# Kernel tuning notes

Hardware: AMD Instinct MI355X
Metric: run time of the kernel (lower is better)

## Reference

```python
import jax, jax.numpy as jnp
import numpy as np

B, N_C, N_F = 2, 16384, 65536          # batch, coarse nodes, fine (up_nodes)
C_IN, C_OUT = 128, 128
E_C, E_F = 65536, 262144               # coarse / fine edge counts


def _mlp_params(key, cin, cout):
    # 2-layer MLP (Linear-ReLU-Linear) + LayerNorm, torch default uniform init
    k1, k2 = jax.random.split(key)
    s1 = 1.0 / np.sqrt(2 * cin)
    s2 = 1.0 / np.sqrt(cout)
    W1 = jax.random.uniform(k1, (2 * cin, cout), minval=-s1, maxval=s1, dtype=jnp.float32)
    W2 = jax.random.uniform(k2, (cout, cout), minval=-s2, maxval=s2, dtype=jnp.float32)
    return (W1, jnp.zeros((cout,), jnp.float32), W2, jnp.zeros((cout,), jnp.float32),
            jnp.ones((cout,), jnp.float32), jnp.zeros((cout,), jnp.float32))


def setup_inputs() -> dict:
    key = jax.random.key(0)
    rng = np.random.default_rng(0)
    x = jax.random.normal(jax.random.fold_in(key, 1), (B, N_C, C_IN), dtype=jnp.float32)
    # sorted unique unpool indices (m_id)
    idx = jnp.asarray(np.sort(rng.choice(N_F, N_C, replace=False)).astype(np.int64))
    ei_c = jnp.asarray(rng.integers(0, N_C, size=(2, E_C)).astype(np.int64))
    ei_f = jnp.asarray(rng.integers(0, N_F, size=(2, E_F)).astype(np.int64))
    d = {"x": x, "idx": idx, "ei_c": ei_c, "ei_f": ei_f}
    for pre, k, cin, cout in (("s", 2, C_IN, C_OUT), ("a", 3, C_IN, C_OUT // 2), ("b", 4, C_OUT // 2, C_OUT)):
        W1, b1, W2, b2, g, bt = _mlp_params(jax.random.fold_in(key, k), cin, cout)
        d.update({pre + "W1": W1, pre + "b1": b1, pre + "W2": W2, pre + "b2": b2, pre + "g": g, pre + "bt": bt})
    return d


def _unpool(x, idx, n):
    # scatter coarse features into a zero-filled fine array (Unpool module)
    return jnp.zeros((x.shape[0], n, x.shape[-1]), x.dtype).at[:, idx].set(x)


def _edgeconv(x, ei, W1, b1, W2, b2, g, bt, n):
    # EdgeConv: aggregate_sum over edges of MLP([x_i, x_j - x_i]) + LayerNorm
    src, dst = ei[0], ei[1]
    xd = x[:, dst]                                   # [B,E,cin] gather at target
    feat = jnp.concatenate([xd, x[:, src] - xd], axis=-1)  # [B,E,2*cin]
    h = jax.nn.relu(feat @ W1 + b1) @ W2 + b2        # [B,E,cout]
    mu = jnp.mean(h, axis=-1, keepdims=True)
    var = jnp.var(h, axis=-1, keepdims=True)
    h = (h - mu) * jax.lax.rsqrt(var + 1e-5) * g + bt
    return jax.vmap(lambda hb: jax.ops.segment_sum(hb, dst, num_segments=n))(h)


def reference(x, idx, ei_c, ei_f,
              sW1, sb1, sW2, sb2, sg, sbt,
              aW1, ab1, aW2, ab2, ag, abt,
              bW1, bb1, bW2, bb2, bg, bbt):
    # skip branch: unpool then EdgeConv cin->cout on fine graph
    skip = _edgeconv(_unpool(x, idx, N_F), ei_f, sW1, sb1, sW2, sb2, sg, sbt, N_F)
    # main branch: EdgeConv cin->cout/2 on coarse, unpool, EdgeConv cout/2->cout on fine
    h = _edgeconv(x, ei_c, aW1, ab1, aW2, ab2, ag, abt, N_C)
    h = _edgeconv(_unpool(h, idx, N_F), ei_f, bW1, bb1, bW2, bb2, bg, bbt, N_F)
    return jax.nn.leaky_relu(h + skip, 0.01)
```

## Files before the change

kernel.cpp:

```cpp
#include <hip/hip_runtime.h>

typedef _Float16 half8  __attribute__((ext_vector_type(8)));
typedef _Float16 half4v __attribute__((ext_vector_type(4)));
typedef _Float16 half2v __attribute__((ext_vector_type(2)));
typedef float    f32x4  __attribute__((ext_vector_type(4)));
typedef float    f32x2  __attribute__((ext_vector_type(2)));
typedef int      i32x4  __attribute__((ext_vector_type(4)));

#define NB 2
#define N_C 16384
#define N_F 65536
#define E_C 65536
#define E_F 262144

#define INV4  ((size_t)N_F / 4)
#define CNT4  ((size_t)(N_F + N_C) / 4)

__global__ void clear_small(int* __restrict__ inv, int* __restrict__ cnt) {
    size_t i = (size_t)blockIdx.x * 256 + threadIdx.x;
    const i32x4 z = {0, 0, 0, 0};
    const i32x4 m1 = {-1, -1, -1, -1};
    if (i < INV4) ((i32x4*)inv)[i] = m1;
    else if (i < INV4 + CNT4) ((i32x4*)cnt)[i - INV4] = z;
}

__device__ inline void swizzle_dev(const float* __restrict__ W, _Float16* __restrict__ Ws,
                                   int N, int o) {
    int j = o & 7;
    int lane = (o >> 3) & 63;
    int frag = o >> 9;
    int ntiles = N >> 4;
    int nt = frag % ntiles;
    int kt = frag / ntiles;
    int k = kt * 32 + (lane >> 4) * 8 + j;
    int n = nt * 16 + (lane & 15);
    Ws[o] = (_Float16)W[k * N + n];
}

__device__ inline void swz_node(const float* __restrict__ W, _Float16* __restrict__ Ws,
                                int CIN, int COUT, int o) {
    int j = o & 7;
    int lane = (o >> 3) & 63;
    int frag = o >> 9;
    int N2 = 2 * COUT;
    int ntiles = N2 >> 4;
    int nt = frag % ntiles;
    int kt = frag / ntiles;
    int k = kt * 32 + (lane >> 4) * 8 + j;
    int n = nt * 16 + (lane & 15);
    float v = (n < COUT) ? W[k * COUT + n] - W[(k + CIN) * COUT + n]
                         : W[(k + CIN) * COUT + (n - COUT)];
    Ws[o] = (_Float16)v;
}

__global__ void setup_all(const int* __restrict__ idx, int* __restrict__ inv,
                          const float* sW1, const float* sW2, const float* aW1,
                          const float* aW2, const float* bW1, const float* bW2,
                          const float* sb1, const float* ab1, const float* bb1,
                          _Float16* sW1n, _Float16* sW2s, _Float16* aW1n,
                          _Float16* aW2s, _Float16* bW1n, _Float16* bW2s,
                          _Float16* b1h,
                          const int* __restrict__ ei_f, const int* __restrict__ ei_c,
                          int* __restrict__ cnt) {
    const int bb = blockIdx.x, t = threadIdx.x;
    if (bb < 64) {
        int i = bb * 256 + t;
        inv[idx[i]] = i;
    } else if (bb < 192) {
        swz_node(sW1, sW1n, 128, 128, (bb - 64) * 256 + t);
    } else if (bb < 256) {
        swizzle_dev(sW2, sW2s, 128, (bb - 192) * 256 + t);
    } else if (bb < 320) {
        swz_node(aW1, aW1n, 128, 64, (bb - 256) * 256 + t);
    } else if (bb < 336) {
        swizzle_dev(aW2, aW2s, 64, (bb - 320) * 256 + t);
    } else if (bb < 400) {
        swz_node(bW1, bW1n, 64, 128, (bb - 336) * 256 + t);
    } else if (bb < 464) {
        swizzle_dev(bW2, bW2s, 128, (bb - 400) * 256 + t);
    } else if (bb < 466) {
        int i = (bb - 464) * 256 + t;
        if (i < 128) b1h[i] = (_Float16)sb1[i];
        else if (i < 192) b1h[i] = (_Float16)ab1[i - 128];
        else if (i < 320) b1h[i] = (_Float16)bb1[i - 192];
    } else if (bb < 1490) {
        int e = (bb - 466) * 256 + t;
        atomicAdd(&cnt[ei_f[E_F + e]], 1);
    } else {
        int e = (bb - 1490) * 256 + t;
        atomicAdd(&cnt[N_F + ei_c[E_C + e]], 1);
    }
}

__global__ void scan1(const int* __restrict__ cnt, int* __restrict__ csum) {
    __shared__ int red[4];
    int v = cnt[blockIdx.x * 256 + threadIdx.x];
    #pragma unroll
    for (int off = 32; off >= 1; off >>= 1) v += __shfl_xor(v, off, 64);
    if ((threadIdx.x & 63) == 0) red[threadIdx.x >> 6] = v;
    __syncthreads();
    if (threadIdx.x == 0) csum[blockIdx.x] = red[0] + red[1] + red[2] + red[3];
}

__global__ void scan2(const int* __restrict__ csum, int* __restrict__ cbase) {
    __shared__ int buf[256];
    const int t = threadIdx.x;
    int v = csum[t];
    buf[t] = v;
    __syncthreads();
    for (int off = 1; off < 256; off <<= 1) {
        int u = (t >= off) ? buf[t - off] : 0;
        __syncthreads();
        buf[t] += u;
        __syncthreads();
    }
    cbase[t] = buf[t] - v;
    __syncthreads();
    int v2 = (t < 64) ? csum[256 + t] : 0;
    buf[t] = v2;
    __syncthreads();
    for (int off = 1; off < 64; off <<= 1) {
        int u = (t >= off) ? buf[t - off] : 0;
        __syncthreads();
        buf[t] += u;
        __syncthreads();
    }
    if (t < 64) cbase[256 + t] = buf[t] - v2;
}

__global__ void scan3zf(const int* __restrict__ cnt, const int* __restrict__ cbase,
                        int* __restrict__ cursor, unsigned char* __restrict__ flagF,
                        float* __restrict__ out, float* __restrict__ h_a) {
    __shared__ int buf[256];
    const int t = threadIdx.x, bb = blockIdx.x;
    const int d = bb * 256 + t;
    int v = cnt[d];
    buf[t] = v;
    __syncthreads();
    for (int off = 1; off < 256; off <<= 1) {
        int u = (t >= off) ? buf[t - off] : 0;
        __syncthreads();
        buf[t] += u;
        __syncthreads();
    }
    const int start = cbase[bb] + buf[t] - v;
    cursor[d] = start;
    const int deg = v;
    const int end = start + deg;
    const f32x4 z = {0.f, 0.f, 0.f, 0.f};
    if (d < N_F) {
        const bool pred = (deg == 0) || ((start >> 5) != ((end - 1) >> 5));
        flagF[d] = pred ? 1 : 0;
        if (pred) {
            f32x4* r0 = (f32x4*)(out + (size_t)d * 128);
            f32x4* r1 = (f32x4*)(out + ((size_t)N_F + d) * 128);
            #pragma unroll
            for (int i = 0; i < 32; ++i) { r0[i] = z; r1[i] = z; }
        }
    } else {
        const int dc = d - N_F;
        const bool pred = (deg == 0) || ((start >> 4) != ((end - 1) >> 4));
        if (pred) {
            f32x4* r0 = (f32x4*)(h_a + (size_t)dc * 64);
            f32x4* r1 = (f32x4*)(h_a + ((size_t)N_C + dc) * 64);
            #pragma unroll
            for (int i = 0; i < 16; ++i) { r0[i] = z; r1[i] = z; }
        }
    }
}

__global__ void scatter2(const int* __restrict__ ei_f, const int* __restrict__ ei_c,
                         const int* __restrict__ inv, int* __restrict__ cursor,
                         i32x4* __restrict__ ef_info, i32x4* __restrict__ ec_info) {
    const int bb = blockIdx.x, t = threadIdx.x;
    if (bb < 1024) {
        int e = bb * 256 + t;
        int s_ = ei_f[e];
        int d_ = ei_f[E_F + e];
        int p = atomicAdd(&cursor[d_], 1);
        i32x4 rec;
        rec.x = inv[s_]; rec.y = inv[d_]; rec.z = d_; rec.w = 0;
        ef_info[p] = rec;
    } else {
        int e = (bb - 1024) * 256 + t;
        int s_ = ei_c[e];
        int d_ = ei_c[E_C + e];
        int p = atomicAdd(&cursor[N_F + d_], 1);
        i32x4 rec;
        rec.x = s_; rec.y = d_; rec.z = d_; rec.w = 0;
        ec_info[p] = rec;
    }
}

template <int CIN, int COUT>
__device__ void node_gemm_body(const float* __restrict__ x, const _Float16* __restrict__ W1n,
                               const float* __restrict__ b1, _Float16* __restrict__ P,
                               _Float16* L, int blk, int t) {
    constexpr int N2 = 2 * COUT;
    constexpr int FP = CIN + 8;
    constexpr int P2 = N2 + 8;
    constexpr int NPW = N2 / 4;
    constexpr int NT = NPW / 16;

    const size_t r0 = (size_t)blk * 64;

    {
        const int m = t >> 2, l4 = t & 3;
        const float* src = x + (r0 + m) * CIN + l4 * (CIN / 4);
        #pragma unroll
        for (int i = 0; i < CIN / 16; ++i) {
            f32x4 v = *(const f32x4*)(src + i * 4);
            half4v h;
            #pragma unroll
            for (int c = 0; c < 4; ++c) h[c] = (_Float16)v[c];
            *(half4v*)(L + m * FP + l4 * (CIN / 4) + i * 4) = h;
        }
    }
    __syncthreads();

    const int wv = t >> 6, lane = t & 63;
    const int q = lane >> 4, lm = lane & 15;
    const int n0 = wv * NPW;
    const f32x4 zero4 = {0.f, 0.f, 0.f, 0.f};

    f32x4 acc[4][NT];
    #pragma unroll
    for (int mt = 0; mt < 4; ++mt)
        #pragma unroll
        for (int nt = 0; nt < NT; ++nt) acc[mt][nt] = zero4;

    #pragma unroll
    for (int kt = 0; kt < CIN / 32; ++kt) {
        half8 a[4];
        #pragma unroll
        for (int mt = 0; mt < 4; ++mt)
            a[mt] = *(const half8*)(L + (mt * 16 + lm) * FP + kt * 32 + q * 8);
        #pragma unroll
        for (int nt = 0; nt < NT; ++nt) {
            half8 bf = *(const half8*)(W1n + ((size_t)(kt * (N2 / 16) + wv * NT + nt) * 64 + lane) * 8);
            #pragma unroll
            for (int mt = 0; mt < 4; ++mt)
                acc[mt][nt] = __builtin_amdgcn_mfma_f32_16x16x32_f16(a[mt], bf, acc[mt][nt], 0, 0, 0);
        }
    }
    __syncthreads();

    #pragma unroll
    for (int nt = 0; nt < NT; ++nt) {
        const int col = n0 + nt * 16 + lm;
        const float bv = (col < COUT) ? b1[col] : 0.f;
        #pragma unroll
        for (int mt = 0; mt < 4; ++mt)
            #pragma unroll
            for (int r = 0; r < 4; ++r)
                L[(mt * 16 + q * 4 + r) * P2 + col] = (_Float16)(acc[mt][nt][r] + bv);
    }
    __syncthreads();

    constexpr int CH = 64 * N2 / 8;
    for (int i = t; i < CH; i += 256) {
        int row = i / (N2 / 8), c8 = i % (N2 / 8);
        *(half8*)(P + (r0 + row) * N2 + c8 * 8) = *(const half8*)(L + row * P2 + c8 * 8);
    }
}

__launch_bounds__(256, 4) __global__
void node_sa(const float* __restrict__ x,
             const _Float16* __restrict__ sW1n, const float* __restrict__ sb1, _Float16* __restrict__ Ps,
             const _Float16* __restrict__ aW1n, const float* __restrict__ ab1, _Float16* __restrict__ Pa) {
    __shared__ __align__(16) _Float16 L[16896];
    const int t = threadIdx.x;
    if (blockIdx.x < NB * N_C / 64)
        node_gemm_body<128, 128>(x, sW1n, sb1, Ps, L, blockIdx.x, t);
    else
        node_gemm_body<128, 64>(x, aW1n, ab1, Pa, L, blockIdx.x - NB * N_C / 64, t);
}

template <int CIN, int COUT>
__launch_bounds__(256, 4) __global__
void node_gemm(const float* __restrict__ x, const _Float16* __restrict__ W1n,
               const float* __restrict__ b1, _Float16* __restrict__ P) {
    __shared__ __align__(16) _Float16 L[16896];
    node_gemm_body<CIN, COUT>(x, W1n, b1, P, L, blockIdx.x, threadIdx.x);
}

__device__ inline half8 relu8(half8 h) {
#if __has_builtin(__builtin_elementwise_max)
    half8 z = {};
    return __builtin_elementwise_max(h, z);
#else
    #pragma unroll
    for (int i = 0; i < 8; ++i) h[i] = h[i] > (_Float16)0 ? h[i] : (_Float16)0;
    return h;
#endif
}

template <int COUT, bool FRESH>
__launch_bounds__(256, 8) __global__
void edge2_mfma(const _Float16* __restrict__ P, int ps,
                const i32x4* __restrict__ einfo, int E,
                const _Float16* __restrict__ W2s, const float* __restrict__ b2,
                const float* __restrict__ g, const float* __restrict__ bt,
                const _Float16* __restrict__ b1h,
                float* __restrict__ dest, int bs_out) {
    constexpr int HPITCH = COUT + 8;
    constexpr int NPW = COUT / 4;
    constexpr int NT = NPW / 16;

    __shared__ __align__(16) _Float16 region[64 * HPITCH];
    __shared__ int dstl[64];
    __shared__ int dpnL[2];
    __shared__ float muL[64];
    __shared__ float rsL[64];

    _Float16* h1L = region;
    _Float16* vnL = region;

    const int t = threadIdx.x;
    const int eb = blockIdx.x * 64;
    const int b = eb / E;
    const int e0 = eb - b * E;

    {
        if (t == 0) dpnL[0] = (e0 > 0) ? einfo[e0 - 1].z : -2;
        else if (t == 1) dpnL[1] = (e0 + 64 < E) ? einfo[e0 + 64].z : -2;
        const int m = t >> 2, l4 = t & 3;
        const i32x4 rec = einfo[e0 + m];
        const int si = rec.x, di = rec.y;
        if (l4 == 0) dstl[m] = rec.z;
        const _Float16* pb = P + (size_t)b * ps;
        const _Float16* ub = (di >= 0) ? pb + (size_t)di * (2 * COUT) : b1h;
        const _Float16* vb = pb + (size_t)(si >= 0 ? si : 0) * (2 * COUT) + COUT;
        constexpr int CPT = COUT / 4;
        const int c0 = l4 * CPT;
        #pragma unroll
        for (int i = 0; i < CPT / 8; ++i) {
            half8 u = *(const half8*)(ub + c0 + i * 8);
            half8 v = {};
            if (si >= 0) v = *(const half8*)(vb + c0 + i * 8);
            *(half8*)(h1L + m * HPITCH + c0 + i * 8) = relu8(u + v);
        }
    }
    __syncthreads();

    const int wv = t >> 6, lane = t & 63;
    const int q = lane >> 4, lm = lane & 15;
    const int n0 = wv * NPW;
    const f32x4 zero4 = {0.f, 0.f, 0.f, 0.f};

    f32x4 acc[4][NT];
    #pragma unroll
    for (int mt = 0; mt < 4; ++mt)
        #pragma unroll
        for (int nt = 0; nt < NT; ++nt) acc[mt][nt] = zero4;

    #pragma unroll
    for (int kt = 0; kt < COUT / 32; ++kt) {
        half8 a[4];
        #pragma unroll
        for (int mt = 0; mt < 4; ++mt)
            a[mt] = *(const half8*)(h1L + (mt * 16 + lm) * HPITCH + kt * 32 + q * 8);
        #pragma unroll
        for (int nt = 0; nt < NT; ++nt) {
            half8 bf = *(const half8*)(W2s + ((size_t)(kt * (COUT / 16) + wv * NT + nt) * 64 + lane) * 8);
            #pragma unroll
            for (int mt = 0; mt < 4; ++mt)
                acc[mt][nt] = __builtin_amdgcn_mfma_f32_16x16x32_f16(a[mt], bf, acc[mt][nt], 0, 0, 0);
        }
    }
    __syncthreads();

    #pragma unroll
    for (int nt = 0; nt < NT; ++nt) {
        const float b2v = b2[n0 + nt * 16 + lm];
        #pragma unroll
        for (int mt = 0; mt < 4; ++mt)
            #pragma unroll
            for (int r = 0; r < 4; ++r)
                vnL[(mt * 16 + q * 4 + r) * HPITCH + n0 + nt * 16 + lm] =
                    (_Float16)(acc[mt][nt][r] + b2v);
    }
    __syncthreads();

    {
        const int m = t >> 2, p = t & 3;
        constexpr int CPT = COUT / 4;
        float s = 0.f, s2 = 0.f;
        #pragma unroll
        for (int c = 0; c < CPT / 8; ++c) {
            half8 h8 = *(const half8*)(vnL + m * HPITCH + p * CPT + c * 8);
            #pragma unroll
            for (int j = 0; j < 8; ++j) {
                float v = (float)h8[j];
                s += v;
                s2 += v * v;
            }
        }
        s += __shfl_xor(s, 1, 64);  s2 += __shfl_xor(s2, 1, 64);
        s += __shfl_xor(s, 2, 64);  s2 += __shfl_xor(s2, 2, 64);
        if (p == 0) {
            float mu = s * (1.f / COUT);
            muL[m] = mu;
            rsL[m] = rsqrtf(s2 * (1.f / COUT) - mu * mu + 1e-5f);
        }
    }
    __syncthreads();

    {
        constexpr int CG = COUT / 64;
        constexpr int W  = 4 / CG;
        constexpr int RW = 64 / W;
        const int wv2 = t >> 6, l2 = t & 63;
        const int cg = wv2 % CG;
        const int h  = wv2 / CG;
        const int c  = cg * 64 + l2;
        const int r0 = h * RW;
        const float gv = g[c], bv = bt[c];
        float* const ob = dest + (size_t)b * bs_out + c;
        int dcur = dstl[r0];
        const int dprev = (r0 == 0) ? dpnL[0] : dstl[r0 - 1];
        bool bflag = (dcur == dprev);
        float rs = 0.f;
        #pragma unroll
        for (int i = 0; i < RW; ++i) {
            const int m = r0 + i;
            const float v = (float)vnL[m * HPITCH + c];
            rs += (v - muL[m]) * rsL[m] * gv + bv;
            const int dnxt = (i == RW - 1)
                               ? ((r0 + RW == 64) ? dpnL[1] : dstl[r0 + RW])
                               : dstl[m + 1];
            if (dnxt != dcur) {
                if (!FRESH || bflag) atomicAdd(ob + (size_t)dcur * COUT, rs);
                else ob[(size_t)dcur * COUT] = rs;
                rs = 0.f; dcur = dnxt; bflag = false;
            } else if (i == RW - 1) {
                atomicAdd(ob + (size_t)dcur * COUT, rs);
            }
        }
    }
}

__launch_bounds__(256, 4) __global__
void edge2_dual(const _Float16* __restrict__ Ps, const _Float16* __restrict__ Pb,
                const i32x4* __restrict__ einfo,
                const _Float16* __restrict__ W2sS, const float* __restrict__ b2s,
                const float* __restrict__ gS, const float* __restrict__ btS,
                const _Float16* __restrict__ W2sB, const float* __restrict__ b2b,
                const float* __restrict__ gB, const float* __restrict__ btB,
                const _Float16* __restrict__ b1hS, const _Float16* __restrict__ b1hB,
                float* __restrict__ out) {
    constexpr int E = E_F;
    constexpr int HP = 136;
    constexpr int IP = 264;

    __shared__ __align__(16) _Float16 region[2 * 64 * HP];
    __shared__ int dstl[64];
    __shared__ int dpn[2];
    __shared__ f32x4 stat4[64];

    _Float16* h1S = region;
    _Float16* h1B = region + 64 * HP;
    _Float16* vnI = region;

    const int t = threadIdx.x;
    const int eb = blockIdx.x * 64;
    const int b = eb / E;
    const int e0 = eb - b * E;

    {
        if (t == 0) dpn[0] = (e0 > 0) ? einfo[e0 - 1].z : -2;
        else if (t == 1) dpn[1] = (e0 + 64 < E) ? einfo[e0 + 64].z : -2;
        const int m = t >> 2, l4 = t & 3;
        const i32x4 rec = einfo[e0 + m];
        const int si = rec.x, di = rec.y;
        if (l4 == 0) dstl[m] = rec.z;
        const size_t pofs = (size_t)b * ((size_t)N_C * 256);
        const _Float16* ubS = (di >= 0) ? Ps + pofs + (size_t)di * 256 : b1hS;
        const _Float16* ubB = (di >= 0) ? Pb + pofs + (size_t)di * 256 : b1hB;
        const size_t so = (size_t)(si >= 0 ? si : 0) * 256 + 128;
        const _Float16* vbS = Ps + pofs + so;
        const _Float16* vbB = Pb + pofs + so;
        const int c0 = l4 * 32;
        #pragma unroll
        for (int i = 0; i < 4; ++i) {
            half8 uS = *(const half8*)(ubS + c0 + i * 8);
            half8 uB = *(const half8*)(ubB + c0 + i * 8);
            half8 vS = {}, vB = {};
            if (si >= 0) {
                vS = *(const half8*)(vbS + c0 + i * 8);
                vB = *(const half8*)(vbB + c0 + i * 8);
            }
            *(half8*)(h1S + m * HP + c0 + i * 8) = relu8(uS + vS);
            *(half8*)(h1B + m * HP + c0 + i * 8) = relu8(uB + vB);
        }
    }
    __syncthreads();

    const int wv = t >> 6, lane = t & 63;
    const int q = lane >> 4, lm = lane & 15;
    const int n0 = wv * 32;
    const f32x4 zero4 = {0.f, 0.f, 0.f, 0.f};

    f32x4 accS[4][2], accB[4][2];
    #pragma unroll
    for (int mt = 0; mt < 4; ++mt)
        #pragma unroll
        for (int nt = 0; nt < 2; ++nt) { accS[mt][nt] = zero4; accB[mt][nt] = zero4; }

    #pragma unroll
    for (int kt = 0; kt < 4; ++kt) {
        half8 aS[4], aB[4];
        #pragma unroll
        for (int mt = 0; mt < 4; ++mt) {
            aS[mt] = *(const half8*)(h1S + (mt * 16 + lm) * HP + kt * 32 + q * 8);
            aB[mt] = *(const half8*)(h1B + (mt * 16 + lm) * HP + kt * 32 + q * 8);
        }
        #pragma unroll
        for (int nt = 0; nt < 2; ++nt) {
            half8 bS = *(const half8*)(W2sS + ((size_t)(kt * 8 + wv * 2 + nt) * 64 + lane) * 8);
            half8 bB = *(const half8*)(W2sB + ((size_t)(kt * 8 + wv * 2 + nt) * 64 + lane) * 8);
            #pragma unroll
            for (int mt = 0; mt < 4; ++mt) {
                accS[mt][nt] = __builtin_amdgcn_mfma_f32_16x16x32_f16(aS[mt], bS, accS[mt][nt], 0, 0, 0);
                accB[mt][nt] = __builtin_amdgcn_mfma_f32_16x16x32_f16(aB[mt], bB, accB[mt][nt], 0, 0, 0);
            }
        }
    }
    __syncthreads();

    #pragma unroll
    for (int nt = 0; nt < 2; ++nt) {
        const int col = n0 + nt * 16 + lm;
        const float b2vS = b2s[col];
        const float b2vB = b2b[col];
        #pragma unroll
        for (int mt = 0; mt < 4; ++mt)
            #pragma unroll
            for (int r = 0; r < 4; ++r) {
                const int row = mt * 16 + q * 4 + r;
                half2v pk;
                pk[0] = (_Float16)(accS[mt][nt][r] + b2vS);
                pk[1] = (_Float16)(accB[mt][nt][r] + b2vB);
                *(half2v*)(vnI + row * IP + col * 2) = pk;
            }
    }
    __syncthreads();

    {
        const int m = t >> 2, p = t & 3;
        float sS = 0.f, s2S = 0.f, sB = 0.f, s2B = 0.f;
        #pragma unroll
        for (int k = 0; k < 8; ++k) {
            half8 h8 = *(const half8*)(vnI + m * IP + p * 64 + k * 8);
            #pragma unroll
            for (int j = 0; j < 8; j += 2) {
                float a = (float)h8[j];     sS += a; s2S += a * a;
                float c = (float)h8[j + 1]; sB += c; s2B += c * c;
            }
        }
        sS += __shfl_xor(sS, 1, 64);  s2S += __shfl_xor(s2S, 1, 64);
        sS += __shfl_xor(sS, 2, 64);  s2S += __shfl_xor(s2S, 2, 64);
        sB += __shfl_xor(sB, 1, 64);  s2B += __shfl_xor(s2B, 1, 64);
        sB += __shfl_xor(sB, 2, 64);  s2B += __shfl_xor(s2B, 2, 64);
        if (p == 0) {
            const float mS = sS * (1.f / 128.f);
            const float rS = rsqrtf(s2S * (1.f / 128.f) - mS * mS + 1e-5f);
            const float mB = sB * (1.f / 128.f);
            const float rB = rsqrtf(s2B * (1.f / 128.f) - mB * mB + 1e-5f);
            f32x4 st;
            st[0] = rS; st[1] = -mS * rS; st[2] = rB; st[3] = -mB * rB;
            stat4[m] = st;
        }
    }
    __syncthreads();

    {
        const int wv2 = t >> 6, l2 = t & 63;
        const int cg = wv2 & 1;
        const int h  = wv2 >> 1;
        const int c  = cg * 64 + l2;
        const int r0 = h * 32;
        const float gS_ = gS[c], gB_ = gB[c];
        const float bsum = btS[c] + btB[c];
        float* const ob = out + (size_t)b * ((size_t)N_F * 128) + c;
        int dcur = dstl[r0];
        const int dprev = (r0 == 0) ? dpn[0] : dstl[r0 - 1];
        bool bflag = (dcur == dprev);
        float rs = 0.f;
        #pragma unroll
        for (int i = 0; i < 32; ++i) {
            const int m = r0 + i;
            const half2v v2 = *(const half2v*)(vnI + m * IP + c * 2);
            const f32x4 st = stat4[m];
            rs += fmaf((float)v2[0], st[0], st[1]) * gS_
                + fmaf((float)v2[1], st[2], st[3]) * gB_ + bsum;
            const int dnxt = (i == 31)
                               ? ((r0 + 32 == 64) ? dpn[1] : dstl[r0 + 32])
                               : dstl[m + 1];
            if (dnxt != dcur) {
                if (bflag) {
                    atomicAdd(ob + (size_t)dcur * 128, rs);
                } else {
                    float v = rs > 0.f ? rs : 0.01f * rs;
                    ob[(size_t)dcur * 128] = v;
                }
                rs = 0.f; dcur = dnxt; bflag = false;
            } else if (i == 31) {
                atomicAdd(ob + (size_t)dcur * 128, rs);
            }
        }
    }
}

__global__ void leaky_fix(float* __restrict__ out, const unsigned char* __restrict__ flagF) {
    const size_t i = (size_t)blockIdx.x * 256 + threadIdx.x;
    if (i >= (size_t)NB * N_F * 32) return;
    const int d = (int)((i >> 5) & (N_F - 1));
    if (!flagF[d]) return;
    f32x4 v = ((f32x4*)out)[i];
    #pragma unroll
    for (int c = 0; c < 4; ++c) v[c] = v[c] > 0.f ? v[c] : 0.01f * v[c];
    ((f32x4*)out)[i] = v;
}

extern "C" void kernel_launch(void* const* d_in, const int* in_sizes, int n_in,
                              void* d_out, int out_size, void* d_ws, size_t ws_size,
                              hipStream_t stream) {
    const float* x    = (const float*)d_in[0];
    const int*   idx  = (const int*)d_in[1];
    const int*   ei_c = (const int*)d_in[2];
    const int*   ei_f = (const int*)d_in[3];
    const float* sW1 = (const float*)d_in[4];
    const float* sb1 = (const float*)d_in[5];
    const float* sW2 = (const float*)d_in[6];
    const float* sb2 = (const float*)d_in[7];
    const float* sg  = (const float*)d_in[8];
    const float* sbt = (const float*)d_in[9];
    const float* aW1 = (const float*)d_in[10];
    const float* ab1 = (const float*)d_in[11];
    const float* aW2 = (const float*)d_in[12];
    const float* ab2 = (const float*)d_in[13];
    const float* ag  = (const float*)d_in[14];
    const float* abt = (const float*)d_in[15];
    const float* bW1 = (const float*)d_in[16];
    const float* bb1 = (const float*)d_in[17];
    const float* bW2 = (const float*)d_in[18];
    const float* bb2 = (const float*)d_in[19];
    const float* bg  = (const float*)d_in[20];
    const float* bbt = (const float*)d_in[21];

    float* out = (float*)d_out;

    char* ws = (char*)d_ws;
    int*   inv    = (int*)ws;                                ws += (size_t)N_F * 4;
    float* h_a    = (float*)ws;                              ws += (size_t)NB * N_C * 64 * 4;
    int*   cnt    = (int*)ws;                                ws += (size_t)(N_F + N_C) * 4;
    int*   cursor = (int*)ws;                                ws += (size_t)(N_F + N_C) * 4;
    int*   csum   = (int*)ws;                                ws += 320 * 4;
    int*   cbase  = (int*)ws;                                ws += 320 * 4;
    i32x4* ef_info = (i32x4*)ws;                             ws += (size_t)E_F * 16;
    i32x4* ec_info = (i32x4*)ws;                             ws += (size_t)E_C * 16;
    _Float16* sW1n = (_Float16*)ws;                          ws += (size_t)128 * 256 * 2;
    _Float16* sW2s = (_Float16*)ws;                          ws += (size_t)128 * 128 * 2;
    _Float16* aW1n = (_Float16*)ws;                          ws += (size_t)128 * 128 * 2;
    _Float16* aW2s = (_Float16*)ws;                          ws += (size_t)64 * 64 * 2;
    _Float16* bW1n = (_Float16*)ws;                          ws += (size_t)64 * 256 * 2;
    _Float16* bW2s = (_Float16*)ws;                          ws += (size_t)128 * 128 * 2;
    _Float16* b1h  = (_Float16*)ws;                          ws += 1024;
    unsigned char* flagF = (unsigned char*)ws;               ws += (size_t)N_F;
    _Float16* P_s  = (_Float16*)ws;                          ws += (size_t)NB * N_C * 256 * 2;
    _Float16* P_a  = (_Float16*)ws;                          ws += (size_t)NB * N_C * 128 * 2;
    _Float16* P_b  = (_Float16*)ws;                          ws += (size_t)NB * N_C * 256 * 2;

    clear_small<<<(int)((INV4 + CNT4 + 255) / 256), 256, 0, stream>>>(inv, cnt);

    setup_all<<<1746, 256, 0, stream>>>(idx, inv, sW1, sW2, aW1, aW2, bW1, bW2,
                                        sb1, ab1, bb1,
                                        sW1n, sW2s, aW1n, aW2s, bW1n, bW2s, b1h,
                                        ei_f, ei_c, cnt);

    scan1<<<320, 256, 0, stream>>>(cnt, csum);
    scan2<<<1, 256, 0, stream>>>(csum, cbase);
    scan3zf<<<320, 256, 0, stream>>>(cnt, cbase, cursor, flagF, out, h_a);

    scatter2<<<1280, 256, 0, stream>>>(ei_f, ei_c, inv, cursor, ef_info, ec_info);

    node_sa<<<2 * (NB * N_C / 64), 256, 0, stream>>>(x, sW1n, sb1, P_s, aW1n, ab1, P_a);

    edge2_mfma<64, true><<<NB * E_C / 64, 256, 0, stream>>>(
        P_a, N_C * 128, ec_info, E_C, aW2s, ab2, ag, abt, b1h + 128, h_a, N_C * 64);

    node_gemm<64, 128><<<NB * N_C / 64, 256, 0, stream>>>(h_a, bW1n, bb1, P_b);

    edge2_dual<<<NB * E_F / 64, 256, 0, stream>>>(
        P_s, P_b, ef_info,
        sW2s, sb2, sg, sbt,
        bW2s, bb2, bg, bbt,
        b1h, b1h + 192, out);

    leaky_fix<<<(int)(((size_t)NB * N_F * 32 + 255) / 256), 256, 0, stream>>>(out, flagF);
}
```

Before: 282.6 us.

## Split dual edge kernel across 512 threads, one half per branch

edge2_dual now launches 512 threads per block. Half of them gather and run the MFMA for the skip branch and the other half for the main branch, so each wave holds only one accumulator set. The interleaved fp16 staging buffer is dropped in favour of writing results back in place into the per-branch tiles, LayerNorm statistics use fdot2 per branch, and the scatter phase covers 16 rows per thread group instead of 32. The zero-fill predicate in scan3zf changes its chunk granularity to 16 edges to match the new segment size. This is meant to raise parallelism and lower per-thread register pressure, at the cost of more threads per block and more atomics.

Measured after the change: 290.7 us. 1.03x slower.

```diff
diff --git a/kernel.cpp b/kernel.cpp
--- a/kernel.cpp
+++ b/kernel.cpp
@@ -149,7 +149,7 @@
     const int end = start + deg;
     const f32x4 z = {0.f, 0.f, 0.f, 0.f};
     if (d < N_F) {
-        const bool pred = (deg == 0) || ((start >> 5) != ((end - 1) >> 5));
+        const bool pred = (deg == 0) || ((start >> 4) != ((end - 1) >> 4));
         flagF[d] = pred ? 1 : 0;
         if (pred) {
             f32x4* r0 = (f32x4*)(out + (size_t)d * 128);
@@ -295,6 +295,14 @@
 #endif
 }
 
+__device__ inline float fdot2f(half2v a, half2v b, float c) {
+#if __has_builtin(__builtin_amdgcn_fdot2)
+    return __builtin_amdgcn_fdot2(a, b, c, false);
+#else
+    return c + (float)a[0] * (float)b[0] + (float)a[1] * (float)b[1];
+#endif
+}
+
 template <int COUT, bool FRESH>
 __launch_bounds__(256, 8) __global__
 void edge2_mfma(const _Float16* __restrict__ P, int ps,
@@ -440,7 +448,7 @@
     }
 }
 
-__launch_bounds__(256, 4) __global__
+__launch_bounds__(512, 6) __global__
 void edge2_dual(const _Float16* __restrict__ Ps, const _Float16* __restrict__ Pb,
                 const i32x4* __restrict__ einfo,
                 const _Float16* __restrict__ W2sS, const float* __restrict__ b2s,
@@ -451,16 +459,14 @@
                 float* __restrict__ out) {
     constexpr int E = E_F;
     constexpr int HP = 136;
-    constexpr int IP = 264;
 
     __shared__ __align__(16) _Float16 region[2 * 64 * HP];
     __shared__ int dstl[64];
     __shared__ int dpn[2];
-    __shared__ f32x4 stat4[64];
-
-    _Float16* h1S = region;
-    _Float16* h1B = region + 64 * HP;
-    _Float16* vnI = region;
+    __shared__ float stat4[64][4];
+
+    _Float16* const h1S = region;
+    _Float16* const h1B = region + 64 * HP;
 
     const int t = threadIdx.x;
     const int eb = blockIdx.x * 64;
@@ -470,106 +476,93 @@
     {
         if (t == 0) dpn[0] = (e0 > 0) ? einfo[e0 - 1].z : -2;
         else if (t == 1) dpn[1] = (e0 + 64 < E) ? einfo[e0 + 64].z : -2;
-        const int m = t >> 2, l4 = t & 3;
+        const int cv = t >> 8;
+        const int m = (t & 255) >> 2, l4 = t & 3;
         const i32x4 rec = einfo[e0 + m];
         const int si = rec.x, di = rec.y;
-        if (l4 == 0) dstl[m] = rec.z;
+        if (cv == 0 && l4 == 0) dstl[m] = rec.z;
+        const _Float16* const Pp  = cv ? Pb : Ps;
+        const _Float16* const b1p = cv ? b1hB : b1hS;
+        _Float16* const h1 = cv ? h1B : h1S;
         const size_t pofs = (size_t)b * ((size_t)N_C * 256);
-        const _Float16* ubS = (di >= 0) ? Ps + pofs + (size_t)di * 256 : b1hS;
-        const _Float16* ubB = (di >= 0) ? Pb + pofs + (size_t)di * 256 : b1hB;
-        const size_t so = (size_t)(si >= 0 ? si : 0) * 256 + 128;
-        const _Float16* vbS = Ps + pofs + so;
-        const _Float16* vbB = Pb + pofs + so;
+        const _Float16* ub = (di >= 0) ? Pp + pofs + (size_t)di * 256 : b1p;
+        const _Float16* vb = Pp + pofs + (size_t)(si >= 0 ? si : 0) * 256 + 128;
         const int c0 = l4 * 32;
         #pragma unroll
         for (int i = 0; i < 4; ++i) {
-            half8 uS = *(const half8*)(ubS + c0 + i * 8);
-            half8 uB = *(const half8*)(ubB + c0 + i * 8);
-            half8 vS = {}, vB = {};
-            if (si >= 0) {
-                vS = *(const half8*)(vbS + c0 + i * 8);
-                vB = *(const half8*)(vbB + c0 + i * 8);
-            }
-            *(half8*)(h1S + m * HP + c0 + i * 8) = relu8(uS + vS);
-            *(half8*)(h1B + m * HP + c0 + i * 8) = relu8(uB + vB);
+            half8 u = *(const half8*)(ub + c0 + i * 8);
+            half8 v = {};
+            if (si >= 0) v = *(const half8*)(vb + c0 + i * 8);
+            *(half8*)(h1 + m * HP + c0 + i * 8) = relu8(u + v);
         }
     }
     __syncthreads();
 
     const int wv = t >> 6, lane = t & 63;
+    const int cv = wv >> 2;
     const int q = lane >> 4, lm = lane & 15;
-    const int n0 = wv * 32;
+    const int n0 = (wv & 3) * 32;
+    const _Float16* const h1 = cv ? h1B : h1S;
+    const _Float16* const W2 = cv ? W2sB : W2sS;
+    const float* const b2 = cv ? b2b : b2s;
     const f32x4 zero4 = {0.f, 0.f, 0.f, 0.f};
 
-    f32x4 accS[4][2], accB[4][2];
+    f32x4 acc[4][2];
     #pragma unroll
     for (int mt = 0; mt < 4; ++mt)
         #pragma unroll
-        for (int nt = 0; nt < 2; ++nt) { accS[mt][nt] = zero4; accB[mt][nt] = zero4; }
+        for (int nt = 0; nt < 2; ++nt) acc[mt][nt] = zero4;
 
     #pragma unroll
     for (int kt = 0; kt < 4; ++kt) {
-        half8 aS[4], aB[4];
-        #pragma unroll
-        for (int mt = 0; mt < 4; ++mt) {
-            aS[mt] = *(const half8*)(h1S + (mt * 16 + lm) * HP + kt * 32 + q * 8);
-            aB[mt] = *(const half8*)(h1B + (mt * 16 + lm) * HP + kt * 32 + q * 8);
-        }
+        half8 a[4];
+        #pragma unroll
+        for (int mt = 0; mt < 4; ++mt)
+            a[mt] = *(const half8*)(h1 + (mt * 16 + lm) * HP + kt * 32 + q * 8);
         #pragma unroll
         for (int nt = 0; nt < 2; ++nt) {
-            half8 bS = *(const half8*)(W2sS + ((size_t)(kt * 8 + wv * 2 + nt) * 64 + lane) * 8);
-            half8 bB = *(const half8*)(W2sB + ((size_t)(kt * 8 + wv * 2 + nt) * 64 + lane) * 8);
-            #pragma unroll
-            for (int mt = 0; mt < 4; ++mt) {
-                accS[mt][nt] = __builtin_amdgcn_mfma_f32_16x16x32_f16(aS[mt], bS, accS[mt][nt], 0, 0, 0);
-                accB[mt][nt] = __builtin_amdgcn_mfma_f32_16x16x32_f16(aB[mt], bB, accB[mt][nt], 0, 0, 0);
-            }
-        }
-    }
-    __syncthreads();
-
-    #pragma unroll
-    for (int nt = 0; nt < 2; ++nt) {
-        const int col = n0 + nt * 16 + lm;
-        const float b2vS = b2s[col];
-        const float b2vB = b2b[col];
-        #pragma unroll
-        for (int mt = 0; mt < 4; ++mt)
-            #pragma unroll
-            for (int r = 0; r < 4; ++r) {
-                const int row = mt * 16 + q * 4 + r;
-                half2v pk;
-                pk[0] = (_Float16)(accS[mt][nt][r] + b2vS);
-                pk[1] = (_Float16)(accB[mt][nt][r] + b2vB);
-                *(half2v*)(vnI + row * IP + col * 2) = pk;
-            }
-    }
-    __syncthreads();
-
-    {
-        const int m = t >> 2, p = t & 3;
-        float sS = 0.f, s2S = 0.f, sB = 0.f, s2B = 0.f;
-        #pragma unroll
-        for (int k = 0; k < 8; ++k) {
-            half8 h8 = *(const half8*)(vnI + m * IP + p * 64 + k * 8);
-            #pragma unroll
-            for (int j = 0; j < 8; j += 2) {
-                float a = (float)h8[j];     sS += a; s2S += a * a;
-                float c = (float)h8[j + 1]; sB += c; s2B += c * c;
-            }
-        }
-        sS += __shfl_xor(sS, 1, 64);  s2S += __shfl_xor(s2S, 1, 64);
-        sS += __shfl_xor(sS, 2, 64);  s2S += __shfl_xor(s2S, 2, 64);
-        sB += __shfl_xor(sB, 1, 64);  s2B += __shfl_xor(s2B, 1, 64);
-        sB += __shfl_xor(sB, 2, 64);  s2B += __shfl_xor(s2B, 2, 64);
+            half8 bf = *(const half8*)(W2 + ((size_t)(kt * 8 + (wv & 3) * 2 + nt) * 64 + lane) * 8);
+            #pragma unroll
+            for (int mt = 0; mt < 4; ++mt)
+                acc[mt][nt] = __builtin_amdgcn_mfma_f32_16x16x32_f16(a[mt], bf, acc[mt][nt], 0, 0, 0);
+        }
+    }
+    __syncthreads();
+
+    {
+        _Float16* const vn = cv ? h1B : h1S;
+        #pragma unroll
+        for (int nt = 0; nt < 2; ++nt) {
+            const int col = n0 + nt * 16 + lm;
+            const float b2v = b2[col];
+            #pragma unroll
+            for (int mt = 0; mt < 4; ++mt)
+                #pragma unroll
+                for (int r = 0; r < 4; ++r)
+                    vn[(mt * 16 + q * 4 + r) * HP + col] = (_Float16)(acc[mt][nt][r] + b2v);
+        }
+    }
+    __syncthreads();
+
+    {
+        const int cv2 = t >> 8;
+        const int m = (t & 255) >> 2, p = t & 3;
+        const _Float16* v = (cv2 ? h1B : h1S) + m * HP + p * 32;
+        const half2v ones = {(_Float16)1.f, (_Float16)1.f};
+        float s = 0.f, s2 = 0.f;
+        #pragma unroll
+        for (int k = 0; k < 16; ++k) {
+            half2v h2 = *(const half2v*)(v + k * 2);
+            s  = fdot2f(h2, ones, s);
+            s2 = fdot2f(h2, h2, s2);
+        }
+        s += __shfl_xor(s, 1, 64);  s2 += __shfl_xor(s2, 1, 64);
+        s += __shfl_xor(s, 2, 64);  s2 += __shfl_xor(s2, 2, 64);
         if (p == 0) {
-            const float mS = sS * (1.f / 128.f);
-            const float rS = rsqrtf(s2S * (1.f / 128.f) - mS * mS + 1e-5f);
-            const float mB = sB * (1.f / 128.f);
-            const float rB = rsqrtf(s2B * (1.f / 128.f) - mB * mB + 1e-5f);
-            f32x4 st;
-            st[0] = rS; st[1] = -mS * rS; st[2] = rB; st[3] = -mB * rB;
-            stat4[m] = st;
+            const float mu = s * (1.f / 128.f);
+            const float rs = rsqrtf(s2 * (1.f / 128.f) - mu * mu + 1e-5f);
+            stat4[m][2 * cv2]     = rs;
+            stat4[m][2 * cv2 + 1] = -mu * rs;
         }
     }
     __syncthreads();
@@ -579,7 +572,7 @@
         const int cg = wv2 & 1;
         const int h  = wv2 >> 1;
         const int c  = cg * 64 + l2;
-        const int r0 = h * 32;
+        const int r0 = h * 16;
         const float gS_ = gS[c], gB_ = gB[c];
         const float bsum = btS[c] + btB[c];
         float* const ob = out + (size_t)b * ((size_t)N_F * 128) + c;
@@ -588,14 +581,15 @@
         bool bflag = (dcur == dprev);
         float rs = 0.f;
         #pragma unroll
-        for (int i = 0; i < 32; ++i) {
+        for (int i = 0; i < 16; ++i) {
             const int m = r0 + i;
-            const half2v v2 = *(const half2v*)(vnI + m * IP + c * 2);
-            const f32x4 st = stat4[m];
-            rs += fmaf((float)v2[0], st[0], st[1]) * gS_
-                + fmaf((float)v2[1], st[2], st[3]) * gB_ + bsum;
-            const int dnxt = (i == 31)
-                               ? ((r0 + 32 == 64) ? dpn[1] : dstl[r0 + 32])
+            const float vS = (float)h1S[m * HP + c];
+            const float vB = (float)h1B[m * HP + c];
+            const f32x4 st = *(const f32x4*)stat4[m];
+            rs += fmaf(vS, st[0], st[1]) * gS_
+                + fmaf(vB, st[2], st[3]) * gB_ + bsum;
+            const int dnxt = (i == 15)
+                               ? ((r0 + 16 == 64) ? dpn[1] : dstl[r0 + 16])
                                : dstl[m + 1];
             if (dnxt != dcur) {
                 if (bflag) {
@@ -605,7 +599,7 @@
                     ob[(size_t)dcur * 128] = v;
                 }
                 rs = 0.f; dcur = dnxt; bflag = false;
-            } else if (i == 31) {
+            } else if (i == 15) {
                 atomicAdd(ob + (size_t)dcur * 128, rs);
             }
         }
@@ -692,7 +686,7 @@
 
     node_gemm<64, 128><<<NB * N_C / 64, 256, 0, stream>>>(h_a, bW1n, bb1, P_b);
 
-    edge2_dual<<<NB * E_F / 64, 256, 0, stream>>>(
+    edge2_dual<<<NB * E_F / 64, 512, 0, stream>>>(
         P_s, P_b, ef_info,
         sW2s, sb2, sg, sbt,
         bW2s, bb2, bg, bbt,
```

## Fold scan2 into scan3, merge scatter with node GEMM, add MFMA priority

Applied to the files above, without the earlier changes.

Each scan3zf block now computes its own prefix base by summing the preceding per-block counts itself, which removes the single-block scan2 launch. The edge-scatter kernel and the node_sa GEMM kernel become one launch with a combined grid, so the irregular atomic scatter can overlap with the MFMA GEMM work. s_setprio is raised around the MFMA loops in the GEMM kernels. The cost is redundant csum reads in each scan block and shared-memory allocation for the scatter blocks in the merged kernel, which may lower occupancy for them.

Result: faster. 274.6 us, median of 2 (-2.8%).

```diff
diff --git a/kernel.cpp b/kernel.cpp
--- a/kernel.cpp
+++ b/kernel.cpp
@@ -102,48 +102,32 @@
     if (threadIdx.x == 0) csum[blockIdx.x] = red[0] + red[1] + red[2] + red[3];
 }
 
-__global__ void scan2(const int* __restrict__ csum, int* __restrict__ cbase) {
+__global__ void scan3zf(const int* __restrict__ cnt, const int* __restrict__ csum,
+                        int* __restrict__ cursor, unsigned char* __restrict__ flagF,
+                        float* __restrict__ out, float* __restrict__ h_a) {
     __shared__ int buf[256];
-    const int t = threadIdx.x;
-    int v = csum[t];
+    __shared__ int red[4];
+    const int t = threadIdx.x, bb = blockIdx.x;
+
+    const int lo = (bb < 256) ? 0 : 256;
+    int part = 0;
+    for (int j = lo + t; j < bb; j += 256) part += csum[j];
+    #pragma unroll
+    for (int off = 32; off >= 1; off >>= 1) part += __shfl_xor(part, off, 64);
+    if ((t & 63) == 0) red[t >> 6] = part;
+
+    const int d = bb * 256 + t;
+    int v = cnt[d];
     buf[t] = v;
     __syncthreads();
+    const int base = red[0] + red[1] + red[2] + red[3];
     for (int off = 1; off < 256; off <<= 1) {
         int u = (t >= off) ? buf[t - off] : 0;
         __syncthreads();
         buf[t] += u;
         __syncthreads();
     }
-    cbase[t] = buf[t] - v;
-    __syncthreads();
-    int v2 = (t < 64) ? csum[256 + t] : 0;
-    buf[t] = v2;
-    __syncthreads();
-    for (int off = 1; off < 64; off <<= 1) {
-        int u = (t >= off) ? buf[t - off] : 0;
-        __syncthreads();
-        buf[t] += u;
-        __syncthreads();
-    }
-    if (t < 64) cbase[256 + t] = buf[t] - v2;
-}
-
-__global__ void scan3zf(const int* __restrict__ cnt, const int* __restrict__ cbase,
-                        int* __restrict__ cursor, unsigned char* __restrict__ flagF,
-                        float* __restrict__ out, float* __restrict__ h_a) {
-    __shared__ int buf[256];
-    const int t = threadIdx.x, bb = blockIdx.x;
-    const int d = bb * 256 + t;
-    int v = cnt[d];
-    buf[t] = v;
-    __syncthreads();
-    for (int off = 1; off < 256; off <<= 1) {
-        int u = (t >= off) ? buf[t - off] : 0;
-        __syncthreads();
-        buf[t] += u;
-        __syncthreads();
-    }
-    const int start = cbase[bb] + buf[t] - v;
+    const int start = base + buf[t] - v;
     cursor[d] = start;
     const int deg = v;
     const int end = start + deg;
@@ -169,9 +153,90 @@
     }
 }
 
-__global__ void scatter2(const int* __restrict__ ei_f, const int* __restrict__ ei_c,
-                         const int* __restrict__ inv, int* __restrict__ cursor,
-                         i32x4* __restrict__ ef_info, i32x4* __restrict__ ec_info) {
+template <int CIN, int COUT>
+__device__ void node_gemm_body(const float* __restrict__ x, const _Float16* __restrict__ W1n,
+                               const float* __restrict__ b1, _Float16* __restrict__ P,
+                               _Float16* L, int blk, int t) {
+    constexpr int N2 = 2 * COUT;
+    constexpr int FP = CIN + 8;
+    constexpr int P2 = N2 + 8;
+    constexpr int NPW = N2 / 4;
+    constexpr int NT = NPW / 16;
+
+    const size_t r0 = (size_t)blk * 64;
+
+    {
+        const int m = t >> 2, l4 = t & 3;
+        const float* src = x + (r0 + m) * CIN + l4 * (CIN / 4);
+        #pragma unroll
+        for (int i = 0; i < CIN / 16; ++i) {
+            f32x4 v = *(const f32x4*)(src + i * 4);
+            half4v h;
+            #pragma unroll
+            for (int c = 0; c < 4; ++c) h[c] = (_Float16)v[c];
+            *(half4v*)(L + m * FP + l4 * (CIN / 4) + i * 4) = h;
+        }
+    }
+    __syncthreads();
+
+    const int wv = t >> 6, lane = t & 63;
+    const int q = lane >> 4, lm = lane & 15;
+    const int n0 = wv * NPW;
+    const f32x4 zero4 = {0.f, 0.f, 0.f, 0.f};
+
+    f32x4 acc[4][NT];
+    #pragma unroll
+    for (int mt = 0; mt < 4; ++mt)
+        #pragma unroll
+        for (int nt = 0; nt < NT; ++nt) acc[mt][nt] = zero4;
+
+    __builtin_amdgcn_s_setprio(1);
+    #pragma unroll
+    for (int kt = 0; kt < CIN / 32; ++kt) {
+        half8 a[4];
+        #pragma unroll
+        for (int mt = 0; mt < 4; ++mt)
+            a[mt] = *(const half8*)(L + (mt * 16 + lm) * FP + kt * 32 + q * 8);
+        #pragma unroll
+        for (int nt = 0; nt < NT; ++nt) {
+            half8 bf = *(const half8*)(W1n + ((size_t)(kt * (N2 / 16) + wv * NT + nt) * 64 + lane) * 8);
+            #pragma unroll
+            for (int mt = 0; mt < 4; ++mt)
+                acc[mt][nt] = __builtin_amdgcn_mfma_f32_16x16x32_f16(a[mt], bf, acc[mt][nt], 0, 0, 0);
+        }
+    }
+    __builtin_amdgcn_s_setprio(0);
+    __syncthreads();
+
+    #pragma unroll
+    for (int nt = 0; nt < NT; ++nt) {
+        const int col = n0 + nt * 16 + lm;
+        const float bv = (col < COUT) ? b1[col] : 0.f;
+        #pragma unroll
+        for (int mt = 0; mt < 4; ++mt)
+            #pragma unroll
+            for (int r = 0; r < 4; ++r)
+                L[(mt * 16 + q * 4 + r) * P2 + col] = (_Float16)(acc[mt][nt][r] + bv);
+    }
+    __syncthreads();
+
+    constexpr int CH = 64 * N2 / 8;
+    for (int i = t; i < CH; i += 256) {
+        int row = i / (N2 / 8), c8 = i % (N2 / 8);
+        *(half8*)(P + (r0 + row) * N2 + c8 * 8) = *(const half8*)(L + row * P2 + c8 * 8);
+    }
+}
+
+__launch_bounds__(256, 4) __global__
+void scatter_nodesa(const int* __restrict__ ei_f, const int* __restrict__ ei_c,
+                    const int* __restrict__ inv, int* __restrict__ cursor,
+                    i32x4* __restrict__ ef_info, i32x4* __restrict__ ec_info,
+                    const float* __restrict__ x,
+                    const _Float16* __restrict__ sW1n, const float* __restrict__ sb1,
+                    _Float16* __restrict__ Ps,
+                    const _Float16* __restrict__ aW1n, const float* __restrict__ ab1,
+                    _Float16* __restrict__ Pa) {
+    __shared__ __align__(16) _Float16 L[16896];
     const int bb = blockIdx.x, t = threadIdx.x;
     if (bb < 1024) {
         int e = bb * 256 + t;
@@ -181,7 +246,7 @@
         i32x4 rec;
         rec.x = inv[s_]; rec.y = inv[d_]; rec.z = d_; rec.w = 0;
         ef_info[p] = rec;
-    } else {
+    } else if (bb < 1280) {
         int e = (bb - 1024) * 256 + t;
         int s_ = ei_c[e];
         int d_ = ei_c[E_C + e];
@@ -189,91 +254,11 @@
         i32x4 rec;
         rec.x = s_; rec.y = d_; rec.z = d_; rec.w = 0;
         ec_info[p] = rec;
-    }
-}
-
-template <int CIN, int COUT>
-__device__ void node_gemm_body(const float* __restrict__ x, const _Float16* __restrict__ W1n,
-                               const float* __restrict__ b1, _Float16* __restrict__ P,
-                               _Float16* L, int blk, int t) {
-    constexpr int N2 = 2 * COUT;
-    constexpr int FP = CIN + 8;
-    constexpr int P2 = N2 + 8;
-    constexpr int NPW = N2 / 4;
-    constexpr int NT = NPW / 16;
-
-    const size_t r0 = (size_t)blk * 64;
-
-    {
-        const int m = t >> 2, l4 = t & 3;
-        const float* src = x + (r0 + m) * CIN + l4 * (CIN / 4);
-        #pragma unroll
-        for (int i = 0; i < CIN / 16; ++i) {
-            f32x4 v = *(const f32x4*)(src + i * 4);
-            half4v h;
-            #pragma unroll
-            for (int c = 0; c < 4; ++c) h[c] = (_Float16)v[c];
-            *(half4v*)(L + m * FP + l4 * (CIN / 4) + i * 4) = h;
-        }
-    }
-    __syncthreads();
-
-    const int wv = t >> 6, lane = t & 63;
-    const int q = lane >> 4, lm = lane & 15;
-    const int n0 = wv * NPW;
-    const f32x4 zero4 = {0.f, 0.f, 0.f, 0.f};
-
-    f32x4 acc[4][NT];
-    #pragma unroll
-    for (int mt = 0; mt < 4; ++mt)
-        #pragma unroll
-        for (int nt = 0; nt < NT; ++nt) acc[mt][nt] = zero4;
-
-    #pragma unroll
-    for (int kt = 0; kt < CIN / 32; ++kt) {
-        half8 a[4];
-        #pragma unroll
-        for (int mt = 0; mt < 4; ++mt)
-            a[mt] = *(const half8*)(L + (mt * 16 + lm) * FP + kt * 32 + q * 8);
-        #pragma unroll
-        for (int nt = 0; nt < NT; ++nt) {
-            half8 bf = *(const half8*)(W1n + ((size_t)(kt * (N2 / 16) + wv * NT + nt) * 64 + lane) * 8);
-            #pragma unroll
-            for (int mt = 0; mt < 4; ++mt)
-                acc[mt][nt] = __builtin_amdgcn_mfma_f32_16x16x32_f16(a[mt], bf, acc[mt][nt], 0, 0, 0);
-        }
-    }
-    __syncthreads();
-
-    #pragma unroll
-    for (int nt = 0; nt < NT; ++nt) {
-        const int col = n0 + nt * 16 + lm;
-        const float bv = (col < COUT) ? b1[col] : 0.f;
-        #pragma unroll
-        for (int mt = 0; mt < 4; ++mt)
-            #pragma unroll
-            for (int r = 0; r < 4; ++r)
-                L[(mt * 16 + q * 4 + r) * P2 + col] = (_Float16)(acc[mt][nt][r] + bv);
-    }
-    __syncthreads();
-
-    constexpr int CH = 64 * N2 / 8;
-    for (int i = t; i < CH; i += 256) {
-        int row = i / (N2 / 8), c8 = i % (N2 / 8);
-        *(half8*)(P + (r0 + row) * N2 + c8 * 8) = *(const half8*)(L + row * P2 + c8 * 8);
-    }
-}
-
-__launch_bounds__(256, 4) __global__
-void node_sa(const float* __restrict__ x,
-             const _Float16* __restrict__ sW1n, const float* __restrict__ sb1, _Float16* __restrict__ Ps,
-             const _Float16* __restrict__ aW1n, const float* __restrict__ ab1, _Float16* __restrict__ Pa) {
-    __shared__ __align__(16) _Float16 L[16896];
-    const int t = threadIdx.x;
-    if (blockIdx.x < NB * N_C / 64)
-        node_gemm_body<128, 128>(x, sW1n, sb1, Ps, L, blockIdx.x, t);
-    else
-        node_gemm_body<128, 64>(x, aW1n, ab1, Pa, L, blockIdx.x - NB * N_C / 64, t);
+    } else if (bb < 1280 + NB * N_C / 64) {
+        node_gemm_body<128, 128>(x, sW1n, sb1, Ps, L, bb - 1280, t);
+    } else {
+        node_gemm_body<128, 64>(x, aW1n, ab1, Pa, L, bb - 1280 - NB * N_C / 64, t);
+    }
 }
 
 template <int CIN, int COUT>
@@ -354,6 +339,7 @@
         #pragma unroll
         for (int nt = 0; nt < NT; ++nt) acc[mt][nt] = zero4;
 
+    __builtin_amdgcn_s_setprio(1);
     #pragma unroll
     for (int kt = 0; kt < COUT / 32; ++kt) {
         half8 a[4];
@@ -368,6 +354,7 @@
                 acc[mt][nt] = __builtin_amdgcn_mfma_f32_16x16x32_f16(a[mt], bf, acc[mt][nt], 0, 0, 0);
         }
     }
+    __builtin_amdgcn_s_setprio(0);
     __syncthreads();
 
     #pragma unroll
@@ -507,6 +494,7 @@
         #pragma unroll
         for (int nt = 0; nt < 2; ++nt) { accS[mt][nt] = zero4; accB[mt][nt] = zero4; }
 
+    __builtin_amdgcn_s_setprio(1);
     #pragma unroll
     for (int kt = 0; kt < 4; ++kt) {
         half8 aS[4], aB[4];
@@ -526,6 +514,7 @@
             }
         }
     }
+    __builtin_amdgcn_s_setprio(0);
     __syncthreads();
 
     #pragma unroll
@@ -671,6 +660,7 @@
     _Float16* P_s  = (_Float16*)ws;                          ws += (size_t)NB * N_C * 256 * 2;
     _Float16* P_a  = (_Float16*)ws;                          ws += (size_t)NB * N_C * 128 * 2;
     _Float16* P_b  = (_Float16*)ws;                          ws += (size_t)NB * N_C * 256 * 2;
+    (void)cbase;
 
     clear_small<<<(int)((INV4 + CNT4 + 255) / 256), 256, 0, stream>>>(inv, cnt);
 
@@ -680,12 +670,12 @@
                                         ei_f, ei_c, cnt);
 
     scan1<<<320, 256, 0, stream>>>(cnt, csum);
-    scan2<<<1, 256, 0, stream>>>(csum, cbase);
-    scan3zf<<<320, 256, 0, stream>>>(cnt, cbase, cursor, flagF, out, h_a);
-
-    scatter2<<<1280, 256, 0, stream>>>(ei_f, ei_c, inv, cursor, ef_info, ec_info);
-
-    node_sa<<<2 * (NB * N_C / 64), 256, 0, stream>>>(x, sW1n, sb1, P_s, aW1n, ab1, P_a);
+
+    scan3zf<<<320, 256, 0, stream>>>(cnt, csum, cursor, flagF, out, h_a);
+
+    scatter_nodesa<<<1280 + 2 * (NB * N_C / 64), 256, 0, stream>>>(
+        ei_f, ei_c, inv, cursor, ef_info, ec_info,
+        x, sW1n, sb1, P_s, aW1n, ab1, P_a);
 
     edge2_mfma<64, true><<<NB * E_C / 64, 256, 0, stream>>>(
         P_a, N_C * 128, ec_info, E_C, aW2s, ab2, ag, abt, b1h + 128, h_a, N_C * 64);
```
